# Kernel tuning notes

Hardware: AMD Instinct MI355X
Metric: run time of the kernel (lower is better)

## Reference

```python
import jax, jax.numpy as jnp
import numpy as np

IN_C = 128
HIDE_C = 256
HC2 = HIDE_C // 2
OUT_C = 128
WS = 7          # winsize
SCALE = 0.125   # 1/8
EPS = 1e-5      # BatchNorm eps
B, H, W = 32, 112, 112


def setup_inputs() -> dict:
    key = jax.random.key(0)
    ks = jax.random.split(key, 24)
    f32 = jnp.float32

    def w(k, shape):
        return jax.random.normal(k, shape, f32) * 0.05

    def bn_params(k, c):
        k1, k2, k3, k4 = jax.random.split(k, 4)
        gamma = 1.0 + 0.1 * jax.random.normal(k1, (c,), f32)
        beta = 0.1 * jax.random.normal(k2, (c,), f32)
        mean = 0.1 * jax.random.normal(k3, (c,), f32)
        var = jax.random.uniform(k4, (c,), f32, 0.5, 1.5)
        return gamma, beta, mean, var

    x = jax.random.normal(ks[0], (B, IN_C, H, W), f32)
    wq = w(ks[1], (HC2, IN_C))
    gq, bq, mq, vq = bn_params(ks[2], HC2)
    wk = w(ks[3], (HC2, IN_C))
    gk, bk, mk, vk = bn_params(ks[4], HC2)
    wv = w(ks[5], (HIDE_C, IN_C))
    gv, bv, mv, vv = bn_params(ks[6], HIDE_C)
    wo = w(ks[7], (OUT_C, HIDE_C))
    bo = 0.05 * jax.random.normal(ks[8], (OUT_C,), f32)
    go, bbo, mo, vo = bn_params(ks[9], OUT_C)
    return {"x": x,
            "wq": wq, "gq": gq, "bq": bq, "mq": mq, "vq": vq,
            "wk": wk, "gk": gk, "bk": bk, "mk": mk, "vk": vk,
            "wv": wv, "gv": gv, "bv": bv, "mv": mv, "vv": vv,
            "wo": wo, "bo": bo, "go": go, "bbo": bbo, "mo": mo, "vo": vo}


def _conv1x1(x, w):
    # 1x1 conv, stride 1, no bias: pure channel contraction
    return jnp.einsum('bchw,oc->bohw', x, w)


def _bn(x, g, b, m, v):
    # inference-mode BatchNorm2d
    p = lambda a: a[None, :, None, None]
    return p(g) * (x - p(m)) * jax.lax.rsqrt(p(v) + EPS) + p(b)


def _to_windows(t):
    # 'b c (h1 ws1) (w1 ws2) -> b (c ws1 ws2) (h1 w1)'
    b, c, h, w = t.shape
    h1, w1 = h // WS, w // WS
    t = t.reshape(b, c, h1, WS, w1, WS).transpose(0, 1, 3, 5, 2, 4)
    return t.reshape(b, c * WS * WS, h1 * w1)


def _forward(x, wq, gq, bq, mq, vq, wk, gk, bk, mk, vk,
             wv, gv, bv, mv, vv, wo, bo, go, bbo, mo, vo):
    q = _bn(_conv1x1(x, wq), gq, bq, mq, vq)   # [B, HC2, H, W]
    k = _bn(_conv1x1(x, wk), gk, bk, mk, vk)   # [B, HC2, H, W]
    v = _bn(_conv1x1(x, wv), gv, bv, mv, vv)   # [B, HIDE_C, H, W]
    b, _, h, w = q.shape
    h1, w1 = h // WS, w // WS

    qf = _to_windows(q)  # [B, HC2*49, h1*w1]
    kf = _to_windows(k)
    vf = _to_windows(v)  # [B, HIDE_C*49, h1*w1]

    dots = jnp.einsum('bci,bcj->bij', qf, kf) * SCALE   # [B, T, T], T=h1*w1
    attn = jax.nn.softmax(dots, axis=-1)
    out = jnp.einsum('bij,bdj->bid', attn, vf)          # [B, T, HIDE_C*49]

    # 'b (h1 w1) (c1 ws1 ws2) -> b c1 (h1 ws1) (w1 ws2)'
    out = out.reshape(b, h1, w1, HIDE_C, WS, WS).transpose(0, 3, 1, 4, 2, 5)
    out = out.reshape(b, HIDE_C, h, w)

    out = jax.nn.gelu(out, approximate=False)
    out = _conv1x1(out, wo) + bo[None, :, None, None]
    out = _bn(out, go, bbo, mo, vo)
    # dropout is identity in eval; downsample is identity (stride=1, in_c==out_c)
    return jax.nn.gelu(out + x, approximate=False)


def reference(x, wq, gq, bq, mq, vq, wk, gk, bk, mk, vk,
              wv, gv, bv, mv, vv, wo, bo, go, bbo, mo, vo):
    return _forward(x, wq, gq, bq, mq, vq, wk, gk, bk, mk, vk,
                    wv, gv, bv, mv, vv, wo, bo, go, bbo, mo, vo)
```

## Files before the change

kernel.cpp:

```cpp
#include <hip/hip_runtime.h>


typedef unsigned short u16;
typedef unsigned int u32;
typedef short s16x8 __attribute__((ext_vector_type(8)));
typedef float f32x4 __attribute__((ext_vector_type(4)));
typedef u16 u16x8 __attribute__((ext_vector_type(8)));
typedef u16 u16x4 __attribute__((ext_vector_type(4)));

#define EPSV 1e-5f

__device__ __forceinline__ float bf2f(u16 h) {
  u32 u = ((u32)h) << 16;
  return __builtin_bit_cast(float, u);
}
__device__ __forceinline__ u16 f2bf(float f) {
  u32 u = __builtin_bit_cast(u32, f);
  u += 0x7FFFu + ((u >> 16) & 1u);
  return (u16)(u >> 16);
}
__device__ __forceinline__ s16x8 ld8(const u16* p) { return *(const s16x8*)p; }
__device__ __forceinline__ f32x4 mfma_bf16(s16x8 a, s16x8 b, f32x4 c) {
  return __builtin_amdgcn_mfma_f32_16x16x32_bf16(a, b, c, 0, 0, 0);
}
__device__ __forceinline__ float gelu_f(float v) {
  float e = exp2f(-2.3022083f * (v + 0.044715f * v * v * v));
  return v / (1.0f + e);
}

__global__ void k_params(
    const float* __restrict__ gq, const float* __restrict__ bq, const float* __restrict__ mq, const float* __restrict__ vq,
    const float* __restrict__ gk, const float* __restrict__ bk, const float* __restrict__ mk, const float* __restrict__ vk,
    const float* __restrict__ gv, const float* __restrict__ bv, const float* __restrict__ mv, const float* __restrict__ vv,
    const float* __restrict__ bo, const float* __restrict__ go, const float* __restrict__ bbo, const float* __restrict__ mo,
    const float* __restrict__ vo,
    float* __restrict__ sc512, float* __restrict__ sh512, float* __restrict__ sco, float* __restrict__ sho)
{
  const int i = threadIdx.x;
  if (i < 128) {
    const float s = gq[i] * rsqrtf(vq[i] + EPSV);
    sc512[i] = s;
    sh512[i] = bq[i] - mq[i] * s;
    const float so = go[i] * rsqrtf(vo[i] + EPSV);
    sco[i] = so;
    sho[i] = (bo[i] - mo[i]) * so + bbo[i];
  } else if (i < 256) {
    const int c = i - 128;
    const float s = gk[c] * rsqrtf(vk[c] + EPSV);
    sc512[i] = s;
    sh512[i] = bk[c] - mk[c] * s;
  } else if (i < 512) {
    const int c = i - 256;
    const float s = gv[c] * rsqrtf(vv[c] + EPSV);
    sc512[i] = s;
    sh512[i] = bv[c] - mv[c] * s;
  }
}

__global__ void k_wconv(const float* __restrict__ wq, const float* __restrict__ wk,
                        const float* __restrict__ wv, const float* __restrict__ sc512,
                        u16* __restrict__ wfused)
{
  const int idx4 = (blockIdx.x * 256 + threadIdx.x) * 4;
  const int co = idx4 >> 7, c = idx4 & 127;
  const float* src = (co < 128) ? (wq + co * 128 + c)
                   : (co < 256) ? (wk + (co - 128) * 128 + c)
                                : (wv + (co - 256) * 128 + c);
  const float s = sc512[co];
  const float4 v = *(const float4*)src;
  u16x4 r;
  r[0] = f2bf(v.x * s); r[1] = f2bf(v.y * s);
  r[2] = f2bf(v.z * s); r[3] = f2bf(v.w * s);
  *(u16x4*)(wfused + idx4) = r;
}

__global__ __launch_bounds__(256, 4) void k_qkv(
    const float* __restrict__ x, const u16* __restrict__ wfused,
    const float* __restrict__ sh512,
    u16* __restrict__ QW, u16* __restrict__ KW, u16* __restrict__ VW)
{
  __shared__ u16 XT[128 * 128];
  const int b = blockIdx.y;
  const int px0 = blockIdx.x * 128;
  const int t = threadIdx.x;
  const int pxl = t & 127, chalf = (t >> 7) * 64;

  {
    const float* xp = x + (size_t)b * 128u * 12544u + (size_t)chalf * 12544u + (size_t)(px0 + pxl);
    const int sw = (pxl & 15) << 3;
    #pragma unroll 4
    for (int i = 0; i < 16; ++i) {
      const int c = i * 4;
      u16x4 pk;
      pk[0] = f2bf(xp[(size_t)(c + 0) * 12544u]);
      pk[1] = f2bf(xp[(size_t)(c + 1) * 12544u]);
      pk[2] = f2bf(xp[(size_t)(c + 2) * 12544u]);
      pk[3] = f2bf(xp[(size_t)(c + 3) * 12544u]);
      *(u16x4*)&XT[pxl * 128 + ((chalf + c) ^ sw)] = pk;
    }
  }
  __syncthreads();

  const int w = t >> 6, l = t & 63, a15 = l & 15, g = l >> 4;

  s16x8 af[2][4];
  #pragma unroll
  for (int pxt = 0; pxt < 2; ++pxt) {
    const int row = w * 32 + pxt * 16 + a15;
    const int sw = (row & 15) << 3;
    #pragma unroll
    for (int ks = 0; ks < 4; ++ks)
      af[pxt][ks] = *(const s16x8*)&XT[row * 128 + ((ks * 32 + g * 8) ^ sw)];
  }
  __syncthreads();

  const int px = px0 + pxl;
  const int hh = px / 112, ww = px - hh * 112;
  const int h1 = hh / 7, p = hh - h1 * 7;
  const int w1 = ww / 7, q = ww - w1 * 7;
  const int j = h1 * 16 + w1, pq = p * 7 + q;
  u16* const qrow = QW + ((size_t)(b * 256 + j) * 49 + pq) * 128 + chalf;
  u16* const krow = KW + ((size_t)(b * 256 + j) * 49 + pq) * 128 + chalf;
  u16* const vrow = VW + (size_t)(b * 256 + j) * 12544 + pq * 256 + chalf;
  const int swf = (pxl & 15) << 3;

  #pragma unroll 1
  for (int phase = 0; phase < 4; ++phase) {
    s16x8 bcur[4];
    {
      const u16* wrow = wfused + (u32)(phase * 128 + a15) * 128u;
      #pragma unroll
      for (int ks = 0; ks < 4; ++ks) bcur[ks] = ld8(wrow + ks * 32 + g * 8);
    }
    #pragma unroll 1
    for (int cot8 = 0; cot8 < 8; ++cot8) {
      s16x8 bnext[4];
      if (cot8 < 7) {
        const u16* wrow = wfused + (u32)(phase * 128 + (cot8 + 1) * 16 + a15) * 128u;
        #pragma unroll
        for (int ks = 0; ks < 4; ++ks) bnext[ks] = ld8(wrow + ks * 32 + g * 8);
      }
      f32x4 acc[2];
      #pragma unroll
      for (int pxt = 0; pxt < 2; ++pxt) { acc[pxt][0]=0.f; acc[pxt][1]=0.f; acc[pxt][2]=0.f; acc[pxt][3]=0.f; }
      #pragma unroll
      for (int ks = 0; ks < 4; ++ks)
        #pragma unroll
        for (int pxt = 0; pxt < 2; ++pxt)
          acc[pxt] = mfma_bf16(af[pxt][ks], bcur[ks], acc[pxt]);

      const float sh = sh512[phase * 128 + cot8 * 16 + a15];
      const int co = cot8 * 16 + a15;
      #pragma unroll
      for (int pxt = 0; pxt < 2; ++pxt) {
        #pragma unroll
        for (int r = 0; r < 4; ++r) {
          const int prow = w * 32 + pxt * 16 + g * 4 + r;
          XT[prow * 128 + (co ^ ((prow & 15) << 3))] = f2bf(acc[pxt][r] + sh);
        }
      }
      #pragma unroll
      for (int ks = 0; ks < 4; ++ks) bcur[ks] = bnext[ks];
    }
    __syncthreads();
    {
      u16* dst = (phase == 0) ? qrow : (phase == 1) ? krow : vrow + (phase - 2) * 128;
      #pragma unroll
      for (int c8 = 0; c8 < 8; ++c8)
        *(u16x8*)(dst + c8 * 8) = *(const u16x8*)&XT[pxl * 128 + ((chalf + c8 * 8) ^ swf)];
    }
    __syncthreads();
  }
}

__global__ __launch_bounds__(512, 2) void k_dots(
    const u16* __restrict__ QW, const u16* __restrict__ KW, float* __restrict__ Pp)
{
  __shared__ u16 QS[256 * 64];
  __shared__ u16 KS[256 * 64];
  const int b = blockIdx.y, ks = blockIdx.x;
  const int nch = (ks == 7) ? 14 : 12;
  const int t = threadIdx.x;
  const int w = t >> 6, l = t & 63, a15 = l & 15, g = l >> 4;
  const int i0w = (w >> 1) * 64, j0w = (w & 1) * 128;

  f32x4 acc[4][8];
  #pragma unroll
  for (int i = 0; i < 4; ++i)
    #pragma unroll
    for (int j = 0; j < 8; ++j) { acc[i][j][0]=0.f; acc[i][j][1]=0.f; acc[i][j][2]=0.f; acc[i][j][3]=0.f; }

  const int srow = t >> 1;
  const int sgr0 = (t & 1) * 4;
  const size_t kb = (size_t)ks * 768 + (size_t)((t & 1) * 32);
  const u16* qsrc = QW + ((size_t)b * 256 + srow) * 6272 + kb;
  const u16* ksrc = KW + ((size_t)b * 256 + srow) * 6272 + kb;
  u16* qdst = &QS[srow * 64];
  u16* kdst = &KS[srow * 64];
  const int swr = srow & 7;

  for (int ch = 0; ch < nch; ++ch) {
    const int k0 = ch * 64;
    #pragma unroll
    for (int gi = 0; gi < 4; ++gi) {
      const int off = ((sgr0 + gi) ^ swr) << 3;
      *(u16x8*)(qdst + off) = *(const u16x8*)(qsrc + k0 + gi * 8);
      *(u16x8*)(kdst + off) = *(const u16x8*)(ksrc + k0 + gi * 8);
    }
    __syncthreads();
    #pragma unroll
    for (int kk = 0; kk < 2; ++kk) {
      s16x8 af[4], bfr[8];
      #pragma unroll
      for (int i4 = 0; i4 < 4; ++i4) {
        const int ir = i0w + i4 * 16 + a15;
        af[i4] = *(const s16x8*)&QS[ir * 64 + (((kk * 4 + g) ^ (ir & 7)) << 3)];
      }
      #pragma unroll
      for (int j8 = 0; j8 < 8; ++j8) {
        const int jr = j0w + j8 * 16 + a15;
        bfr[j8] = *(const s16x8*)&KS[jr * 64 + (((kk * 4 + g) ^ (jr & 7)) << 3)];
      }
      #pragma unroll
      for (int i4 = 0; i4 < 4; ++i4)
        #pragma unroll
        for (int j8 = 0; j8 < 8; ++j8)
          acc[i4][j8] = mfma_bf16(af[i4], bfr[j8], acc[i4][j8]);
    }
    __syncthreads();
  }

  float* pp = Pp + ((size_t)ks * 32 + b) * 256 * 256;
  #pragma unroll
  for (int i4 = 0; i4 < 4; ++i4)
    #pragma unroll
    for (int r = 0; r < 4; ++r) {
      const int ir = i0w + i4 * 16 + g * 4 + r;
      #pragma unroll
      for (int j8 = 0; j8 < 8; ++j8)
        pp[(size_t)ir * 256 + j0w + j8 * 16 + a15] = acc[i4][j8][r];
    }
}

__global__ __launch_bounds__(256, 4) void k_smax(const float* __restrict__ Pp, u16* __restrict__ P)
{
  const int b = blockIdx.y, it = blockIdx.x;
  const int t = threadIdx.x;
  const int row = it * 32 + (t >> 3);
  const int cg = t & 7;
  const size_t rb = ((size_t)b * 256 + row) * 256 + cg * 32;

  f32x4 s[8];
  #pragma unroll
  for (int cc = 0; cc < 8; ++cc) { s[cc][0]=0.f; s[cc][1]=0.f; s[cc][2]=0.f; s[cc][3]=0.f; }
  #pragma unroll 1
  for (int ks = 0; ks < 8; ++ks) {
    const float* src = Pp + (size_t)ks * 32 * 256 * 256 + rb;
    #pragma unroll
    for (int cc = 0; cc < 8; ++cc)
      s[cc] += *(const f32x4*)(src + cc * 4);
  }
  float m = -1e30f;
  #pragma unroll
  for (int cc = 0; cc < 8; ++cc)
    m = fmaxf(m, fmaxf(fmaxf(s[cc][0], s[cc][1]), fmaxf(s[cc][2], s[cc][3])));
  m = fmaxf(m, __shfl_xor(m, 1));
  m = fmaxf(m, __shfl_xor(m, 2));
  m = fmaxf(m, __shfl_xor(m, 4));
  const float CEXP = 0.18033688f;
  float sum = 0.f;
  #pragma unroll
  for (int cc = 0; cc < 8; ++cc)
    #pragma unroll
    for (int e = 0; e < 4; ++e) {
      const float p = exp2f((s[cc][e] - m) * CEXP);
      s[cc][e] = p;
      sum += p;
    }
  sum += __shfl_xor(sum, 1);
  sum += __shfl_xor(sum, 2);
  sum += __shfl_xor(sum, 4);
  const float inv = 1.0f / sum;
  u16* dst = P + rb;
  #pragma unroll
  for (int cc = 0; cc < 8; cc += 2) {
    u16x8 o;
    o[0] = f2bf(s[cc][0] * inv);     o[1] = f2bf(s[cc][1] * inv);
    o[2] = f2bf(s[cc][2] * inv);     o[3] = f2bf(s[cc][3] * inv);
    o[4] = f2bf(s[cc + 1][0] * inv); o[5] = f2bf(s[cc + 1][1] * inv);
    o[6] = f2bf(s[cc + 1][2] * inv); o[7] = f2bf(s[cc + 1][3] * inv);
    *(u16x8*)(dst + cc * 4) = o;
  }
}

__global__ __launch_bounds__(512, 2) void k_pv(
    const u16* __restrict__ P, const u16* __restrict__ VW, u16* __restrict__ GN)
{
  __shared__ u16 VT[256 * 64];
  __shared__ u16 PS[256 * 64];
  const int b = blockIdx.y, pq = blockIdx.x;
  const int t = threadIdx.x;
  const int w = t >> 6, l = t & 63, a15 = l & 15, g = l >> 4;
  const int m0w = (w >> 1) * 64, i0w = (w & 1) * 128;

  f32x4 acc[4][8];
  #pragma unroll
  for (int i = 0; i < 4; ++i)
    #pragma unroll
    for (int j = 0; j < 8; ++j) { acc[i][j][0]=0.f; acc[i][j][1]=0.f; acc[i][j][2]=0.f; acc[i][j][3]=0.f; }

  const int sj0 = (t & 7) * 8;
  const int sm0 = (t >> 3) * 4;
  const u16* vbase = VW + ((size_t)b * 256 + sj0) * 12544 + pq * 256 + sm0;
  const int prow = t >> 1;
  const int pgr0 = (t & 1) * 4;
  const u16* pbase = P + ((size_t)b * 256 + prow) * 256 + (t & 1) * 32;
  u16* psdst = &PS[prow * 64];
  const int pswr = prow & 7;

  for (int jc = 0; jc < 4; ++jc) {
    const int j0 = jc * 64;
    u16x4 rr[8];
    #pragma unroll
    for (int ji = 0; ji < 8; ++ji)
      rr[ji] = *(const u16x4*)(vbase + (size_t)(j0 + ji) * 12544);
    #pragma unroll
    for (int mi = 0; mi < 4; ++mi) {
      u16x8 wv;
      #pragma unroll
      for (int ji = 0; ji < 8; ++ji) wv[ji] = rr[ji][mi];
      const int m = sm0 + mi;
      *(u16x8*)&VT[m * 64 + (((sj0 >> 3) ^ (m & 7)) << 3)] = wv;
    }
    #pragma unroll
    for (int gi = 0; gi < 4; ++gi) {
      const int off = ((pgr0 + gi) ^ pswr) << 3;
      *(u16x8*)(psdst + off) = *(const u16x8*)(pbase + j0 + gi * 8);
    }
    __syncthreads();
    #pragma unroll
    for (int kk = 0; kk < 2; ++kk) {
      s16x8 av[4], bp[8];
      #pragma unroll
      for (int mf = 0; mf < 4; ++mf) {
        const int m = m0w + mf * 16 + a15;
        av[mf] = *(const s16x8*)&VT[m * 64 + (((kk * 4 + g) ^ (m & 7)) << 3)];
      }
      #pragma unroll
      for (int f = 0; f < 8; ++f) {
        const int i = i0w + f * 16 + a15;
        bp[f] = *(const s16x8*)&PS[i * 64 + (((kk * 4 + g) ^ (i & 7)) << 3)];
      }
      #pragma unroll
      for (int mf = 0; mf < 4; ++mf)
        #pragma unroll
        for (int f = 0; f < 8; ++f)
          acc[mf][f] = mfma_bf16(av[mf], bp[f], acc[mf][f]);
    }
    __syncthreads();
  }

  const int pp_ = pq / 7, qq = pq - 7 * pp_;
  #pragma unroll
  for (int f = 0; f < 8; ++f) {
    const int i = i0w + f * 16 + a15;
    const int h1 = i >> 4, w1 = i & 15;
    const size_t gb = ((size_t)b * 12544 + (size_t)((h1 * 7 + pp_) * 112 + w1 * 7 + qq)) * 256;
    #pragma unroll
    for (int mf = 0; mf < 4; ++mf) {
      u16x4 st;
      #pragma unroll
      for (int r = 0; r < 4; ++r) st[r] = f2bf(gelu_f(acc[mf][f][r]));
      *(u16x4*)&GN[gb + m0w + mf * 16 + g * 4] = st;
    }
  }
}

__global__ __launch_bounds__(512, 2) void k_out(
    const u16* __restrict__ GN, const float* __restrict__ wo,
    const float* __restrict__ x, const float* __restrict__ sco,
    const float* __restrict__ sho, float* __restrict__ out)
{
  __shared__ u16 WO[128 * 256];
  __shared__ u16 OT[128 * 264];
  const int b = blockIdx.y;
  const int px0 = blockIdx.x * 256;
  const int t = threadIdx.x;
  const int w = t >> 6, l = t & 63, a15 = l & 15, g = l >> 4;

  {
    const int o = t >> 2, gr0 = (t & 3) * 8;
    const float s = sco[o];
    const float* src = wo + o * 256 + gr0 * 8;
    u16* dr = &WO[o * 256];
    #pragma unroll
    for (int gi = 0; gi < 8; ++gi) {
      const float4 v0 = *(const float4*)(src + gi * 8);
      const float4 v1 = *(const float4*)(src + gi * 8 + 4);
      u16x8 pk;
      pk[0] = f2bf(v0.x * s); pk[1] = f2bf(v0.y * s);
      pk[2] = f2bf(v0.z * s); pk[3] = f2bf(v0.w * s);
      pk[4] = f2bf(v1.x * s); pk[5] = f2bf(v1.y * s);
      pk[6] = f2bf(v1.z * s); pk[7] = f2bf(v1.w * s);
      *(u16x8*)(dr + (((gr0 + gi) ^ (o & 7)) << 3)) = pk;
    }
  }
  __syncthreads();

  const int pw = w >> 1, ow = w & 1;
  const int o0w = ow * 64;
  f32x4 acc[4][4];
  #pragma unroll
  for (int i = 0; i < 4; ++i)
    #pragma unroll
    for (int j = 0; j < 4; ++j) { acc[i][j][0]=0.f; acc[i][j][1]=0.f; acc[i][j][2]=0.f; acc[i][j][3]=0.f; }

  #pragma unroll 1
  for (int ksl = 0; ksl < 8; ++ksl) {
    s16x8 af[4], bw[4];
    #pragma unroll
    for (int pxf = 0; pxf < 4; ++pxf) {
      const int row = px0 + pw * 64 + pxf * 16 + a15;
      af[pxf] = ld8(GN + ((size_t)b * 12544 + row) * 256 + ksl * 32 + g * 8);
    }
    #pragma unroll
    for (int of = 0; of < 4; ++of) {
      const int o = o0w + of * 16 + a15;
      bw[of] = *(const s16x8*)&WO[o * 256 + (((ksl * 4 + g) ^ (o & 7)) << 3)];
    }
    #pragma unroll
    for (int pxf = 0; pxf < 4; ++pxf)
      #pragma unroll
      for (int of = 0; of < 4; ++of)
        acc[pxf][of] = mfma_bf16(af[pxf], bw[of], acc[pxf][of]);
  }

  #pragma unroll
  for (int pxf = 0; pxf < 4; ++pxf)
    #pragma unroll
    for (int of = 0; of < 4; ++of) {
      u16x4 st;
      #pragma unroll
      for (int r = 0; r < 4; ++r) st[r] = f2bf(acc[pxf][of][r]);
      *(u16x4*)&OT[(o0w + of * 16 + a15) * 264 + pw * 64 + pxf * 16 + g * 4] = st;
    }
  __syncthreads();

  const int o2 = t >> 2;
  const float sh = sho[o2];
  const size_t xb = ((size_t)b * 128 + o2) * 12544 + px0;
  #pragma unroll 2
  for (int ii = 0; ii < 16; ++ii) {
    const int po = ii * 16 + (t & 3) * 4;
    const u16x4 zt = *(const u16x4*)&OT[o2 * 264 + po];
    const float4 xv = *(const float4*)(x + xb + po);
    float4 r;
    r.x = gelu_f(bf2f(zt[0]) + sh + xv.x);
    r.y = gelu_f(bf2f(zt[1]) + sh + xv.y);
    r.z = gelu_f(bf2f(zt[2]) + sh + xv.z);
    r.w = gelu_f(bf2f(zt[3]) + sh + xv.w);
    *(float4*)(out + xb + po) = r;
  }
}

extern "C" void kernel_launch(void* const* d_in, const int* in_sizes, int n_in,
                              void* d_out, int out_size, void* d_ws, size_t ws_size,
                              hipStream_t stream) {
  (void)in_sizes; (void)n_in; (void)out_size; (void)ws_size;
  const float* x   = (const float*)d_in[0];
  const float* wq  = (const float*)d_in[1];
  const float* gq  = (const float*)d_in[2];
  const float* bq  = (const float*)d_in[3];
  const float* mq  = (const float*)d_in[4];
  const float* vq  = (const float*)d_in[5];
  const float* wk  = (const float*)d_in[6];
  const float* gk  = (const float*)d_in[7];
  const float* bk  = (const float*)d_in[8];
  const float* mk  = (const float*)d_in[9];
  const float* vk  = (const float*)d_in[10];
  const float* wv  = (const float*)d_in[11];
  const float* gv  = (const float*)d_in[12];
  const float* bv  = (const float*)d_in[13];
  const float* mv  = (const float*)d_in[14];
  const float* vv  = (const float*)d_in[15];
  const float* wo  = (const float*)d_in[16];
  const float* bo  = (const float*)d_in[17];
  const float* go  = (const float*)d_in[18];
  const float* bbo = (const float*)d_in[19];
  const float* mo  = (const float*)d_in[20];
  const float* vo  = (const float*)d_in[21];

  u16* QW = (u16*)d_ws;
  u16* KW = QW + 51380224u;
  u16* VW = KW + 51380224u;
  u16* GN = VW + 102760448u;
  u16* P  = QW;
  float* Pp = (float*)GN;
  u16* wfused = GN;
  float* sc512 = (float*)(GN + 102760448u);
  float* sh512 = sc512 + 512;
  float* sco = sh512 + 512;
  float* sho = sco + 128;

  k_params<<<1, 512, 0, stream>>>(gq, bq, mq, vq, gk, bk, mk, vk, gv, bv, mv, vv,
                                  bo, go, bbo, mo, vo, sc512, sh512, sco, sho);
  k_wconv<<<64, 256, 0, stream>>>(wq, wk, wv, sc512, wfused);
  k_qkv<<<dim3(98, 32), 256, 0, stream>>>(x, wfused, sh512, QW, KW, VW);
  k_dots<<<dim3(8, 32), 512, 0, stream>>>(QW, KW, Pp);
  k_smax<<<dim3(8, 32), 256, 0, stream>>>(Pp, P);
  k_pv<<<dim3(49, 32), 512, 0, stream>>>(P, VW, GN);
  k_out<<<dim3(49, 32), 512, 0, stream>>>(GN, wo, x, sco, sho, (float*)d_out);
}
```

Before: 775.3 us.

## Add separate transpose kernel producing pixel-major bf16 x for QKV projection

Adds a k_xpose kernel that reads x with float4 loads, converts it to bf16 and writes a pixel-major [B, HW, C] copy into workspace. k_qkv then loads its MFMA A-fragments directly from global memory instead of doing scalar strided fp32 loads and an LDS transpose. The weight-fragment loop is fully unrolled, the software prefetch of the next weight rows is dropped, and the shift values are loaded once per phase. This adds an extra launch and a write-then-read round trip of a bf16 copy of x (about 100 MB) in exchange for coalesced loads and fewer barriers in k_qkv.

```diff
diff --git a/kernel.cpp b/kernel.cpp
--- a/kernel.cpp
+++ b/kernel.cpp
@@ -74,8 +74,42 @@
   *(u16x4*)(wfused + idx4) = r;
 }
 
+__global__ __launch_bounds__(512, 2) void k_xpose(
+    const float* __restrict__ x, u16* __restrict__ XN)
+{
+  __shared__ u16 XT[256 * 128];
+  const int b = blockIdx.y;
+  const int px0 = blockIdx.x * 256;
+  const int t = threadIdx.x;
+  const int pg4 = t & 15, c0 = t >> 4;
+
+  #pragma unroll
+  for (int it = 0; it < 4; ++it) {
+    const int pxb = it * 64 + pg4 * 4;
+    float4 v[4];
+    #pragma unroll
+    for (int cc = 0; cc < 4; ++cc)
+      v[cc] = *(const float4*)(x + ((size_t)b * 128 + c0 * 4 + cc) * 12544 + px0 + pxb);
+    #pragma unroll
+    for (int pp = 0; pp < 4; ++pp) {
+      const int px = pxb + pp;
+      u16x4 pk;
+      pk[0] = f2bf(v[0][pp]); pk[1] = f2bf(v[1][pp]);
+      pk[2] = f2bf(v[2][pp]); pk[3] = f2bf(v[3][pp]);
+      *(u16x4*)&XT[px * 128 + ((c0 * 4) ^ (((px >> 2) & 15) << 3))] = pk;
+    }
+  }
+  __syncthreads();
+  const int px = t >> 1, half = (t & 1) * 64;
+  const int swz = ((px >> 2) & 15) << 3;
+  u16* dst = XN + ((size_t)b * 12544 + px0 + px) * 128 + half;
+  #pragma unroll
+  for (int i = 0; i < 8; ++i)
+    *(u16x8*)(dst + i * 8) = *(const u16x8*)&XT[px * 128 + ((half + i * 8) ^ swz)];
+}
+
 __global__ __launch_bounds__(256, 4) void k_qkv(
-    const float* __restrict__ x, const u16* __restrict__ wfused,
+    const u16* __restrict__ XN, const u16* __restrict__ wfused,
     const float* __restrict__ sh512,
     u16* __restrict__ QW, u16* __restrict__ KW, u16* __restrict__ VW)
 {
@@ -84,35 +118,16 @@
   const int px0 = blockIdx.x * 128;
   const int t = threadIdx.x;
   const int pxl = t & 127, chalf = (t >> 7) * 64;
-
-  {
-    const float* xp = x + (size_t)b * 128u * 12544u + (size_t)chalf * 12544u + (size_t)(px0 + pxl);
-    const int sw = (pxl & 15) << 3;
-    #pragma unroll 4
-    for (int i = 0; i < 16; ++i) {
-      const int c = i * 4;
-      u16x4 pk;
-      pk[0] = f2bf(xp[(size_t)(c + 0) * 12544u]);
-      pk[1] = f2bf(xp[(size_t)(c + 1) * 12544u]);
-      pk[2] = f2bf(xp[(size_t)(c + 2) * 12544u]);
-      pk[3] = f2bf(xp[(size_t)(c + 3) * 12544u]);
-      *(u16x4*)&XT[pxl * 128 + ((chalf + c) ^ sw)] = pk;
-    }
-  }
-  __syncthreads();
-
   const int w = t >> 6, l = t & 63, a15 = l & 15, g = l >> 4;
 
   s16x8 af[2][4];
   #pragma unroll
   for (int pxt = 0; pxt < 2; ++pxt) {
-    const int row = w * 32 + pxt * 16 + a15;
-    const int sw = (row & 15) << 3;
+    const size_t rowb = ((size_t)b * 12544 + px0 + w * 32 + pxt * 16 + a15) * 128;
     #pragma unroll
     for (int ks = 0; ks < 4; ++ks)
-      af[pxt][ks] = *(const s16x8*)&XT[row * 128 + ((ks * 32 + g * 8) ^ sw)];
-  }
-  __syncthreads();
+      af[pxt][ks] = ld8(XN + rowb + ks * 32 + g * 8);
+  }
 
   const int px = px0 + pxl;
   const int hh = px / 112, ww = px - hh * 112;
@@ -126,20 +141,17 @@
 
   #pragma unroll 1
   for (int phase = 0; phase < 4; ++phase) {
-    s16x8 bcur[4];
-    {
-      const u16* wrow = wfused + (u32)(phase * 128 + a15) * 128u;
-      #pragma unroll
-      for (int ks = 0; ks < 4; ++ks) bcur[ks] = ld8(wrow + ks * 32 + g * 8);
-    }
-    #pragma unroll 1
+    float shv[8];
+    #pragma unroll
+    for (int c8 = 0; c8 < 8; ++c8) shv[c8] = sh512[phase * 128 + c8 * 16 + a15];
+
+    #pragma unroll
     for (int cot8 = 0; cot8 < 8; ++cot8) {
-      s16x8 bnext[4];
-      if (cot8 < 7) {
-        const u16* wrow = wfused + (u32)(phase * 128 + (cot8 + 1) * 16 + a15) * 128u;
-        #pragma unroll
-        for (int ks = 0; ks < 4; ++ks) bnext[ks] = ld8(wrow + ks * 32 + g * 8);
-      }
+      s16x8 bfr[4];
+      const u16* wrow = wfused + (u32)(phase * 128 + cot8 * 16 + a15) * 128u;
+      #pragma unroll
+      for (int ks = 0; ks < 4; ++ks) bfr[ks] = ld8(wrow + ks * 32 + g * 8);
+
       f32x4 acc[2];
       #pragma unroll
       for (int pxt = 0; pxt < 2; ++pxt) { acc[pxt][0]=0.f; acc[pxt][1]=0.f; acc[pxt][2]=0.f; acc[pxt][3]=0.f; }
@@ -147,20 +159,17 @@
       for (int ks = 0; ks < 4; ++ks)
         #pragma unroll
         for (int pxt = 0; pxt < 2; ++pxt)
-          acc[pxt] = mfma_bf16(af[pxt][ks], bcur[ks], acc[pxt]);
-
-      const float sh = sh512[phase * 128 + cot8 * 16 + a15];
+          acc[pxt] = mfma_bf16(af[pxt][ks], bfr[ks], acc[pxt]);
+
       const int co = cot8 * 16 + a15;
       #pragma unroll
       for (int pxt = 0; pxt < 2; ++pxt) {
         #pragma unroll
         for (int r = 0; r < 4; ++r) {
           const int prow = w * 32 + pxt * 16 + g * 4 + r;
-          XT[prow * 128 + (co ^ ((prow & 15) << 3))] = f2bf(acc[pxt][r] + sh);
+          XT[prow * 128 + (co ^ ((prow & 15) << 3))] = f2bf(acc[pxt][r] + shv[cot8]);
         }
       }
-      #pragma unroll
-      for (int ks = 0; ks < 4; ++ks) bcur[ks] = bnext[ks];
     }
     __syncthreads();
     {
@@ -497,6 +506,7 @@
   u16* P  = QW;
   float* Pp = (float*)GN;
   u16* wfused = GN;
+  u16* XN = GN + 1048576u;
   float* sc512 = (float*)(GN + 102760448u);
   float* sh512 = sc512 + 512;
   float* sco = sh512 + 512;
@@ -505,7 +515,8 @@
   k_params<<<1, 512, 0, stream>>>(gq, bq, mq, vq, gk, bk, mk, vk, gv, bv, mv, vv,
                                   bo, go, bbo, mo, vo, sc512, sh512, sco, sho);
   k_wconv<<<64, 256, 0, stream>>>(wq, wk, wv, sc512, wfused);
-  k_qkv<<<dim3(98, 32), 256, 0, stream>>>(x, wfused, sh512, QW, KW, VW);
+  k_xpose<<<dim3(49, 32), 512, 0, stream>>>(x, XN);
+  k_qkv<<<dim3(98, 32), 256, 0, stream>>>(XN, wfused, sh512, QW, KW, VW);
   k_dots<<<dim3(8, 32), 512, 0, stream>>>(QW, KW, Pp);
   k_smax<<<dim3(8, 32), 256, 0, stream>>>(Pp, P);
   k_pv<<<dim3(49, 32), 512, 0, stream>>>(P, VW, GN);
```

New measurement: 856.1 us. +10.4%, slower.
